# Optimization experiments

Hardware: AMD Instinct MI355X
Metric: run time of the kernel (lower is better)

The kernel has to match this reference:

```python
import jax, jax.numpy as jnp
import numpy as np

B, T, H, IN, D = 256, 64, 256, 2, 8

def _gru_cell(x, h, Wih, Whh, bih, bhh):
    gi = x @ Wih.T + bih          # [B,3H]
    gh = h @ Whh.T + bhh
    ir, iz, inn = jnp.split(gi, 3, axis=-1)
    hr, hz, hn = jnp.split(gh, 3, axis=-1)
    r = jax.nn.sigmoid(ir + hr)
    z = jax.nn.sigmoid(iz + hz)
    n = jnp.tanh(inn + r * hn)
    return (1.0 - z) * n + z * h

def _gru2(x, h, p):
    # h: [2,B,H]; p: 8-tuple of layer-0 then layer-1 GRU params
    h0 = _gru_cell(x, h[0], p[0], p[1], p[2], p[3])
    h1 = _gru_cell(h0, h[1], p[4], p[5], p[6], p[7])
    return jnp.stack([h0, h1], axis=0)

def _attend(h_new, buf, i, attn_W, v_W, fc_W, fc_b):
    # h_new: [2,B,H] fresh RNN hidden; buf: [B,T,2,H] history of hiddens
    s = h_new.transpose(1, 0, 2)                            # [B,2,H]
    es = jnp.einsum('blh,gh->blg', s, attn_W[:, :H])        # s half of cat(s,hiddens)
    eh = jnp.einsum('bjlh,gh->bjlg', buf, attn_W[:, H:])    # hiddens half
    energy = jnp.tanh(es[:, None] + eh)                     # [B,T,2,H]
    logits = jnp.einsum('bjlg,og->bjlo', energy, v_W)       # [B,T,2,2]
    mask = (jnp.arange(buf.shape[1]) <= i)[None, :, None, None]
    logits = jnp.where(mask, logits, jnp.float32(-1e30))
    m = logits.max(axis=(1, 2), keepdims=True)              # softmax over all 2*(i+1) history slots
    e = jnp.exp(logits - m)
    a = e / e.sum(axis=(1, 2), keepdims=True)
    c = jnp.einsum('bjlo,bjlh->obh', a, buf)                # [2,B,H] == bmm(a,hiddens).transpose(0,1)
    h_cat = jnp.concatenate([c, h_new], axis=-1)            # [2,B,2H]
    return h_cat @ fc_W.T + fc_b                            # [2,B,H]

def setup_inputs():
    key = jax.random.key(0)
    ks = jax.random.split(key, 32)
    def u(k, shape, fan):
        b = 1.0 / np.sqrt(fan)
        return jax.random.uniform(k, shape, jnp.float32, -b, b)
    inp = {'received': jax.random.normal(ks[0], (B, T, IN), jnp.float32)}
    i = 1
    for g in ('g1', 'g2'):
        inp[g + '_Wih0'] = u(ks[i], (3 * H, IN), H); i += 1
        inp[g + '_Whh0'] = u(ks[i], (3 * H, H), H); i += 1
        inp[g + '_bih0'] = u(ks[i], (3 * H,), H); i += 1
        inp[g + '_bhh0'] = u(ks[i], (3 * H,), H); i += 1
        inp[g + '_Wih1'] = u(ks[i], (3 * H, H), H); i += 1
        inp[g + '_Whh1'] = u(ks[i], (3 * H, H), H); i += 1
        inp[g + '_bih1'] = u(ks[i], (3 * H,), H); i += 1
        inp[g + '_bhh1'] = u(ks[i], (3 * H,), H); i += 1
    inp['fc_W'] = u(ks[i], (H, 2 * H), 2 * H); i += 1
    inp['fc_b'] = u(ks[i], (H,), 2 * H); i += 1
    inp['attn_W'] = u(ks[i], (H, 2 * H), 2 * H); i += 1
    inp['v_W'] = u(ks[i], (2, H), H); i += 1
    inp['out_W'] = u(ks[i], (1, 2 * H), 2 * H); i += 1
    inp['out_b'] = u(ks[i], (1,), 2 * H); i += 1
    return inp

def reference(received, g1_Wih0, g1_Whh0, g1_bih0, g1_bhh0, g1_Wih1, g1_Whh1, g1_bih1, g1_bhh1,
              g2_Wih0, g2_Whh0, g2_bih0, g2_bhh0, g2_Wih1, g2_Whh1, g2_bih1, g2_bhh1,
              fc_W, fc_b, attn_W, v_W, out_W, out_b):
    p1 = (g1_Wih0, g1_Whh0, g1_bih0, g1_bhh0, g1_Wih1, g1_Whh1, g1_bih1, g1_bhh1)
    p2 = (g2_Wih0, g2_Whh0, g2_bih0, g2_bhh0, g2_Wih1, g2_Whh1, g2_bih1, g2_bhh1)
    b, t = received.shape[0], received.shape[1]
    h_init = jnp.zeros((2, b, H), received.dtype)
    buf_init = jnp.zeros((b, t, 2, H), received.dtype)

    def step(carry, inp):
        h1, h2, b1, b2 = carry
        x, i = inp
        h1n = _gru2(x, h1, p1)
        h2n = _gru2(x, h2, p2)
        b1 = b1.at[:, i].set(h1n.transpose(1, 0, 2))
        b2 = b2.at[:, i].set(h2n.transpose(1, 0, 2))
        h1a = _attend(h1n, b1, i, attn_W, v_W, fc_W, fc_b)
        h2a = _attend(h2n, b2, i, attn_W, v_W, fc_W, fc_b)
        return (h1a, h2a, b1, b2), (h1n[1], h2n[1])

    xs = (received.transpose(1, 0, 2), jnp.arange(t))
    _, (o1, o2) = jax.lax.scan(step, (h_init, h_init, buf_init, buf_init), xs)
    out1 = o1.transpose(1, 0, 2)   # [B,T,H] = concat of per-step top-layer GRU outputs
    out2 = o2.transpose(1, 0, 2)
    ar = jnp.arange(t)
    idx = jnp.where(ar >= t - D - 1, t - 1, ar + D)   # delayed stream-2 features
    rnn_out = jnp.concatenate([out1, out2[:, idx]], axis=-1)  # [B,T,2H]
    return jax.nn.sigmoid(rnn_out @ out_W.T + out_b)          # [B,T,1]
```

## Files before the change

### kernel.cpp

```cpp
#include <hip/hip_runtime.h>

#define BATCH 256
#define TT    64
#define HH    256
#define DD    8

#define BW    4
#define NTHR  1024
#define NBLK  (2 * (BATCH / BW))

typedef __attribute__((ext_vector_type(8))) short bfrag;
typedef __attribute__((ext_vector_type(4))) float f4;
typedef unsigned int uint_t;
typedef __attribute__((ext_vector_type(4))) unsigned int uv4;

#define SWZ(g) ((((g) & 31) << 3) | ((g) >> 5))

__device__ __forceinline__ float rcpf(float x) { return __builtin_amdgcn_rcpf(x); }
__device__ __forceinline__ float sigf(float x) { return rcpf(1.0f + __expf(-x)); }
__device__ __forceinline__ float tanh_fast(float x) {
  const float e = __expf(-2.0f * x);
  return __builtin_fmaf(2.0f, rcpf(1.0f + e), -1.0f);
}
__device__ __forceinline__ unsigned short f2bf(float f) {
  union { float f; unsigned int u; } v; v.f = f;
  return (unsigned short)((v.u + 0x7fffu + ((v.u >> 16) & 1u)) >> 16);
}
__device__ __forceinline__ float bf_lo(unsigned int u) {
  union { unsigned int u; float f; } v; v.u = u << 16; return v.f;
}
__device__ __forceinline__ float bf_hi(unsigned int u) {
  union { unsigned int u; float f; } v; v.u = u & 0xffff0000u; return v.f;
}
__device__ __forceinline__ bfrag zero_frag() {
  bfrag r;
#pragma unroll
  for (int x = 0; x < 8; x++) r[x] = 0;
  return r;
}
__device__ __forceinline__ f4 mfma16(bfrag a, bfrag b, f4 c) {
  return __builtin_amdgcn_mfma_f32_16x16x32_bf16(a, b, c, 0, 0, 0);
}

#define W1_ELEMS  196608
#define STACK_W   (3 * W1_ELEMS)
#define B3_OFF    (2 * STACK_W)
#define B4_OFF    (B3_OFF + 131072)
#define WF_TOTAL  (B4_OFF + 131072)

__global__ __launch_bounds__(256) void prep_weights(
    const float* __restrict__ g1_Whh0, const float* __restrict__ g1_Wih1, const float* __restrict__ g1_Whh1,
    const float* __restrict__ g2_Whh0, const float* __restrict__ g2_Wih1, const float* __restrict__ g2_Whh1,
    const float* __restrict__ attn_W, const float* __restrict__ fc_W,
    unsigned short* __restrict__ wf) {
  const int id = blockIdx.x * 256 + threadIdx.x;
  if (id >= WF_TOTAL) return;
  float src;
  if (id < 2 * STACK_W) {
    const int s = id / STACK_W, r = id % STACK_W;
    const int mm = r / W1_ELEMS, e = r % W1_ELEMS;
    const int j = e & 7, lane = (e >> 3) & 63, c = (e >> 9) & 7, t = e >> 12;
    const int nt = t / 3, g = t % 3;
    const int n = nt * 16 + (lane & 15);
    const int k = c * 32 + ((lane >> 4) << 3) + j;
    const float* W = (mm == 0) ? (s ? g2_Whh0 : g1_Whh0)
                   : (mm == 1) ? (s ? g2_Wih1 : g1_Wih1)
                               : (s ? g2_Whh1 : g1_Whh1);
    src = W[(g * 256 + n) * 256 + k];
  } else if (id < B4_OFF) {
    const int e = id - B3_OFF;
    const int j = e & 7, lane = (e >> 3) & 63, c = (e >> 9) & 7, t = e >> 12;
    const int n = t * 16 + (lane & 15);
    const int k = c * 32 + ((lane >> 4) << 3) + j;
    src = (n < 256) ? attn_W[n * 512 + k] : attn_W[(n - 256) * 512 + 256 + k];
  } else {
    const int e = id - B4_OFF;
    const int j = e & 7, lane = (e >> 3) & 63, c = (e >> 9) & 15, t = e >> 13;
    const int n = t * 16 + (lane & 15);
    const int k = c * 32 + ((lane >> 4) << 3) + j;
    src = fc_W[n * 512 + k];
  }
  wf[id] = f2bf(src);
}

__global__ __launch_bounds__(NTHR, 4) void gru_attn(
    const float* __restrict__ received,
    const float* __restrict__ g1_Wih0, const float* __restrict__ g1_bih0, const float* __restrict__ g1_bhh0,
    const float* __restrict__ g1_bih1, const float* __restrict__ g1_bhh1,
    const float* __restrict__ g2_Wih0, const float* __restrict__ g2_bih0, const float* __restrict__ g2_bhh0,
    const float* __restrict__ g2_bih1, const float* __restrict__ g2_bhh1,
    const float* __restrict__ fc_b, const float* __restrict__ v_W, const float* __restrict__ out_W,
    const unsigned short* __restrict__ wf,
    unsigned short* __restrict__ buf_g, unsigned short* __restrict__ ehb_g,
    float* __restrict__ ws_p) {
  const int tid  = threadIdx.x;
  const int lane = tid & 63, wave = tid >> 6;
  const int col  = lane & 15, q = lane >> 4;
  const int s    = blockIdx.x & 1;
  const int b0   = (blockIdx.x >> 1) * BW;

  const float* Wih0 = s ? g2_Wih0 : g1_Wih0;
  const float* bih0 = s ? g2_bih0 : g1_bih0;
  const float* bhh0 = s ? g2_bhh0 : g1_bhh0;
  const float* bih1 = s ? g2_bih1 : g1_bih1;
  const float* bhh1 = s ? g2_bhh1 : g1_bhh1;

  const bfrag* W1  = (const bfrag*)(wf + (size_t)s * STACK_W);
  const bfrag* W2I = W1 + W1_ELEMS / 8;
  const bfrag* W2H = W2I + W1_ELEMS / 8;
  const bfrag* B3  = (const bfrag*)(wf + B3_OFF);
  const bfrag* B4  = (const bfrag*)(wf + B4_OFF);

  unsigned short* buf = buf_g + (size_t)s * BATCH * TT * 2 * HH;
  unsigned short* ehb = ehb_g + (size_t)s * BATCH * TT * 2 * HH;
  float* pp = ws_p + (size_t)s * BATCH * TT;

  const int nm = wave * 16 + col;
  const float wxr0 = Wih0[nm * 2],         wxr1 = Wih0[nm * 2 + 1];
  const float wxz0 = Wih0[(256 + nm) * 2], wxz1 = Wih0[(256 + nm) * 2 + 1];
  const float wxn0 = Wih0[(512 + nm) * 2], wxn1 = Wih0[(512 + nm) * 2 + 1];
  const float br0  = bih0[nm] + bhh0[nm];
  const float bz0  = bih0[256 + nm] + bhh0[256 + nm];
  const float bni0 = bih0[512 + nm], bnh0 = bhh0[512 + nm];
  const float br1  = bih1[nm] + bhh1[nm];
  const float bz1  = bih1[256 + nm] + bhh1[256 + nm];
  const float bni1 = bih1[512 + nm], bnh1 = bhh1[512 + nm];
  const float fcbv = fc_b[nm];
  const float owv  = out_W[s * HH + nm];

  __shared__ float          hf[8 * 260] __attribute__((aligned(16)));
  __shared__ unsigned short hb[8 * 264] __attribute__((aligned(16)));
  __shared__ unsigned short hnb[8 * 264] __attribute__((aligned(16)));
  __shared__ float          es_s[8 * 264] __attribute__((aligned(16)));
  __shared__ unsigned short cacb[8 * 264] __attribute__((aligned(16)));
  __shared__ float          lp[TT * 4 * 2 * 2];
  __shared__ float          vw_s[512];
  __shared__ float          cpart[2 * 2 * 4 * 256];
  __shared__ float          pw_s[64];
  __shared__ float          sinv_s[8];

  for (int x = tid; x < 8 * 260; x += NTHR) hf[x] = 0.0f;
  for (int x = tid; x < 8 * 264; x += NTHR) hb[x] = 0;
  if (tid < 512) { const int o = tid >> 8, g = tid & 255; vw_s[o * 256 + SWZ(g)] = v_W[tid]; }
  __syncthreads();

#pragma unroll 1
  for (int i = 0; i < TT; ++i) {
    float2 xv[BW];
#pragma unroll
    for (int b = 0; b < BW; b++) xv[b] = ((const float2*)received)[(size_t)(b0 + b) * TT + i];

    {
      f4 aR = {0, 0, 0, 0}, aZ = {0, 0, 0, 0}, aN = {0, 0, 0, 0};
#pragma unroll
      for (int c = 0; c < 8; c++) {
        const bfrag a = (col < BW) ? *(const bfrag*)&hb[col * 264 + c * 32 + q * 8] : zero_frag();
        aR = mfma16(a, W1[((wave * 3 + 0) * 8 + c) * 64 + lane], aR);
        aZ = mfma16(a, W1[((wave * 3 + 1) * 8 + c) * 64 + lane], aZ);
        aN = mfma16(a, W1[((wave * 3 + 2) * 8 + c) * 64 + lane], aN);
      }
      if (lane < 16) {
#pragma unroll
        for (int reg = 0; reg < 4; reg++) {
          const int b = reg;
          const float r  = sigf(xv[b].x * wxr0 + xv[b].y * wxr1 + br0 + aR[reg]);
          const float z  = sigf(xv[b].x * wxz0 + xv[b].y * wxz1 + bz0 + aZ[reg]);
          const float nn = tanh_fast(xv[b].x * wxn0 + xv[b].y * wxn1 + bni0 + r * (aN[reg] + bnh0));
          const float hn0 = (1.0f - z) * nn + z * hf[b * 260 + nm];
          const unsigned short hv = f2bf(hn0);
          hnb[b * 264 + nm] = hv;
          buf[((size_t)(b0 + b) * (TT * 2) + i * 2 + 0) * HH + nm] = hv;
        }
      }
    }
    __syncthreads();

    {
      f4 iR = {0,0,0,0}, iZ = {0,0,0,0}, iN = {0,0,0,0};
      f4 hR = {0,0,0,0}, hZ = {0,0,0,0}, hN = {0,0,0,0};
#pragma unroll
      for (int c = 0; c < 8; c++) {
        const bfrag ai = (col < BW) ? *(const bfrag*)&hnb[col * 264 + c * 32 + q * 8] : zero_frag();
        const bfrag ah = (col < BW) ? *(const bfrag*)&hb[(4 + col) * 264 + c * 32 + q * 8] : zero_frag();
        iR = mfma16(ai, W2I[((wave * 3 + 0) * 8 + c) * 64 + lane], iR);
        iZ = mfma16(ai, W2I[((wave * 3 + 1) * 8 + c) * 64 + lane], iZ);
        iN = mfma16(ai, W2I[((wave * 3 + 2) * 8 + c) * 64 + lane], iN);
        hR = mfma16(ah, W2H[((wave * 3 + 0) * 8 + c) * 64 + lane], hR);
        hZ = mfma16(ah, W2H[((wave * 3 + 1) * 8 + c) * 64 + lane], hZ);
        hN = mfma16(ah, W2H[((wave * 3 + 2) * 8 + c) * 64 + lane], hN);
      }
      float pv[4] = {0.f, 0.f, 0.f, 0.f};
      if (lane < 16) {
#pragma unroll
        for (int reg = 0; reg < 4; reg++) {
          const int b = reg;
          const float r  = sigf(iR[reg] + hR[reg] + br1);
          const float z  = sigf(iZ[reg] + hZ[reg] + bz1);
          const float nn = tanh_fast(iN[reg] + bni1 + r * (hN[reg] + bnh1));
          const float hn1 = (1.0f - z) * nn + z * hf[(4 + b) * 260 + nm];
          const unsigned short hv = f2bf(hn1);
          hnb[(4 + b) * 264 + nm] = hv;
          buf[((size_t)(b0 + b) * (TT * 2) + i * 2 + 1) * HH + nm] = hv;
          pv[reg] = hn1 * owv;
        }
      }
#pragma unroll
      for (int reg = 0; reg < 4; reg++) {
#pragma unroll
        for (int d = 1; d < 16; d <<= 1) pv[reg] += __shfl_xor(pv[reg], d, 64);
      }
      if (lane == 0) {
#pragma unroll
        for (int reg = 0; reg < 4; reg++) pw_s[wave * 4 + reg] = pv[reg];
      }
    }
    __syncthreads();

    {
#pragma unroll
      for (int tt = 0; tt < 2; tt++) {
        const int t = wave * 2 + tt;
        f4 acc = {0, 0, 0, 0};
#pragma unroll
        for (int c = 0; c < 8; c++) {
          const bfrag a = (col < 8) ? *(const bfrag*)&hnb[col * 264 + c * 32 + q * 8] : zero_frag();
          acc = mfma16(a, B3[(t * 8 + c) * 64 + lane], acc);
        }
        if (lane < 32) {
          const int n = t * 16 + col;
#pragma unroll
          for (int reg = 0; reg < 4; reg++) {
            const int m = q * 4 + reg;
            const int l = m >> 2, b = m & 3;
            if (t < 16) es_s[(b * 2 + l) * 264 + SWZ(n)] = acc[reg];
            else ehb[((size_t)(b0 + b) * (TT * 2) + i * 2 + l) * HH + (n - 256)] = f2bf(acc[reg]);
          }
        }
      }
      if (tid < 4) {
        float ss = 0.0f;
#pragma unroll
        for (int w = 0; w < 16; w++) ss += pw_s[w * 4 + tid];
        pp[(size_t)(b0 + tid) * TT + i] = ss;
      }
    }
    __syncthreads();

    {
      const int nslot = 64 * (i + 1);
      for (int slot = tid; slot < nslot; slot += NTHR) {
        const int g8 = slot & 7;
        const int b  = (slot >> 3) & 3;
        const int l  = (slot >> 5) & 1;
        const int j  = slot >> 6;
        const uv4* ep = (const uv4*)(ehb + ((size_t)(b0 + b) * (TT * 2) + j * 2 + l) * HH + g8 * 32);
        const int eb = (b * 2 + l) * 264;
        float l0 = 0.0f, l1 = 0.0f;
#pragma unroll
        for (int u = 0; u < 4; u++) {
          const uv4 uu = __builtin_nontemporal_load(ep + u);
#pragma unroll
          for (int k = 0; k < 4; k++) {
            const int m = u * 8 + k * 2;
            const float e0 = tanh_fast(es_s[eb + (m * 8 + g8)] + bf_lo(uu[k]));
            const float e1 = tanh_fast(es_s[eb + ((m + 1) * 8 + g8)] + bf_hi(uu[k]));
            l0 = fmaf(e0, vw_s[m * 8 + g8], fmaf(e1, vw_s[(m + 1) * 8 + g8], l0));
            l1 = fmaf(e0, vw_s[256 + m * 8 + g8], fmaf(e1, vw_s[256 + (m + 1) * 8 + g8], l1));
          }
        }
#pragma unroll
        for (int d = 1; d < 8; d <<= 1) { l0 += __shfl_xor(l0, d, 64); l1 += __shfl_xor(l1, d, 64); }
        if (g8 == 0) {
          lp[((j * 4 + b) * 2 + l) * 2 + 0] = __expf(l0);
          lp[((j * 4 + b) * 2 + l) * 2 + 1] = __expf(l1);
        }
      }
    }
    __syncthreads();

    {
      if (wave < 8) {
        const int b = wave >> 1, o = wave & 1;
        float sa = 0.0f;
        if (lane <= i)
          sa = lp[((lane * 4 + b) * 2 + 0) * 2 + o] + lp[((lane * 4 + b) * 2 + 1) * 2 + o];
#pragma unroll
        for (int d = 1; d < 64; d <<= 1) sa += __shfl_xor(sa, d, 64);
        if (lane == 0) sinv_s[b * 2 + o] = rcpf(sa);
      }
      const int b = tid >> 8, jh = (tid >> 7) & 1, h2 = tid & 127;
      const uint_t* bp = (const uint_t*)(buf + ((size_t)(b0 + b) * (TT * 2)) * HH) + h2;
      float c00 = 0.f, c01 = 0.f, c10 = 0.f, c11 = 0.f;
      for (int j = jh; j <= i; j += 2) {
#pragma unroll
        for (int l = 0; l < 2; l++) {
          const uint_t u = __builtin_nontemporal_load(bp + (j * 2 + l) * 128);
          const float e0 = lp[((j * 4 + b) * 2 + l) * 2 + 0];
          const float e1 = lp[((j * 4 + b) * 2 + l) * 2 + 1];
          const float v0 = bf_lo(u), v1 = bf_hi(u);
          c00 = fmaf(e0, v0, c00); c01 = fmaf(e0, v1, c01);
          c10 = fmaf(e1, v0, c10); c11 = fmaf(e1, v1, c11);
        }
      }
      float* cp0 = &cpart[((jh * 2 + 0) * 4 + b) * 256 + h2 * 2];
      cp0[0] = c00; cp0[1] = c01;
      float* cp1 = &cpart[((jh * 2 + 1) * 4 + b) * 256 + h2 * 2];
      cp1[0] = c10; cp1[1] = c11;
    }
    __syncthreads();

    {
#pragma unroll
      for (int r = 0; r < 2; r++) {
        const int idx = tid + r * NTHR;
        const int o = idx >> 10, b = (idx >> 8) & 3, h = idx & 255;
        const float v = (cpart[(o * 4 + b) * 256 + h] + cpart[((2 + o) * 4 + b) * 256 + h]) *
                        sinv_s[b * 2 + o];
        cacb[(o * 4 + b) * 264 + h] = f2bf(v);
      }
    }
    __syncthreads();

    {
      f4 acc = {0, 0, 0, 0};
#pragma unroll
      for (int c = 0; c < 16; c++) {
        bfrag a;
        if (col < 8) {
          if (c < 8) a = *(const bfrag*)&cacb[col * 264 + c * 32 + q * 8];
          else       a = *(const bfrag*)&hnb[col * 264 + (c - 8) * 32 + q * 8];
        } else a = zero_frag();
        acc = mfma16(a, B4[(wave * 16 + c) * 64 + lane], acc);
      }
      if (lane < 32) {
#pragma unroll
        for (int reg = 0; reg < 4; reg++) {
          const int m = q * 4 + reg;
          const float v = acc[reg] + fcbv;
          hf[m * 260 + nm] = v;
          hb[m * 264 + nm] = f2bf(v);
        }
      }
    }
    __syncthreads();
  }
}

__global__ __launch_bounds__(256) void final_combine(const float* __restrict__ ws_p,
                                                     const float* __restrict__ out_b,
                                                     float* __restrict__ out) {
  const int gidx = blockIdx.x * blockDim.x + threadIdx.x;
  if (gidx >= BATCH * TT) return;
  const int b = gidx >> 6;
  const int t = gidx & 63;
  const int idx = (t >= TT - DD - 1) ? (TT - 1) : (t + DD);
  const float* p1 = ws_p;
  const float* p2 = ws_p + (size_t)BATCH * TT;
  const float v = p1[(size_t)b * TT + t] + p2[(size_t)b * TT + idx] + out_b[0];
  out[gidx] = 1.0f / (1.0f + __expf(-v));
}

extern "C" void kernel_launch(void* const* d_in, const int* in_sizes, int n_in,
                              void* d_out, int out_size, void* d_ws, size_t ws_size,
                              hipStream_t stream) {
  const float* received = (const float*)d_in[0];
  const float* g1_Wih0 = (const float*)d_in[1];
  const float* g1_Whh0 = (const float*)d_in[2];
  const float* g1_bih0 = (const float*)d_in[3];
  const float* g1_bhh0 = (const float*)d_in[4];
  const float* g1_Wih1 = (const float*)d_in[5];
  const float* g1_Whh1 = (const float*)d_in[6];
  const float* g1_bih1 = (const float*)d_in[7];
  const float* g1_bhh1 = (const float*)d_in[8];
  const float* g2_Wih0 = (const float*)d_in[9];
  const float* g2_Whh0 = (const float*)d_in[10];
  const float* g2_bih0 = (const float*)d_in[11];
  const float* g2_bhh0 = (const float*)d_in[12];
  const float* g2_Wih1 = (const float*)d_in[13];
  const float* g2_Whh1 = (const float*)d_in[14];
  const float* g2_bih1 = (const float*)d_in[15];
  const float* g2_bhh1 = (const float*)d_in[16];
  const float* fc_W   = (const float*)d_in[17];
  const float* fc_b   = (const float*)d_in[18];
  const float* attn_W = (const float*)d_in[19];
  const float* v_W    = (const float*)d_in[20];
  const float* out_W  = (const float*)d_in[21];
  const float* out_b  = (const float*)d_in[22];

  float* ws_p = (float*)d_ws;
  unsigned short* buf = (unsigned short*)(ws_p + 2 * BATCH * TT);
  unsigned short* ehb = buf + (size_t)2 * BATCH * TT * 2 * HH;
  unsigned short* wf  = ehb + (size_t)2 * BATCH * TT * 2 * HH;

  hipLaunchKernelGGL(prep_weights, dim3((WF_TOTAL + 255) / 256), dim3(256), 0, stream,
                     g1_Whh0, g1_Wih1, g1_Whh1, g2_Whh0, g2_Wih1, g2_Whh1,
                     attn_W, fc_W, wf);

  hipLaunchKernelGGL(gru_attn, dim3(NBLK), dim3(NTHR), 0, stream,
                     received,
                     g1_Wih0, g1_bih0, g1_bhh0, g1_bih1, g1_bhh1,
                     g2_Wih0, g2_bih0, g2_bhh0, g2_bih1, g2_bhh1,
                     fc_b, v_W, out_W, wf, buf, ehb, ws_p);

  hipLaunchKernelGGL(final_combine, dim3((BATCH * TT + 255) / 256), dim3(256), 0, stream,
                     ws_p, out_b, (float*)d_out);
}
```

Measured before the change: 6.185 ms.

## Halve block size, give each wave two tiles, prefetch weights and history loads

Blocks shrink from 1024 to 512 threads, so each wave now covers two output tiles in the GRU, energy and fc stages. The A fragments are hoisted into registers, and all B fragments for a tile are loaded before its MFMAs run. The energy loop and the context accumulation now software-prefetch the next ehb/buf chunk, and the context loop uses wider uv2 loads. The aim is to hide global-load latency and lower barrier cost per wave, at the price of more registers per thread and fewer waves per block.

After: 5.926 ms. -4.2%, faster.

```diff
diff --git a/kernel.cpp b/kernel.cpp
--- a/kernel.cpp
+++ b/kernel.cpp
@@ -6,13 +6,13 @@
 #define DD    8
 
 #define BW    4
-#define NTHR  1024
+#define NTHR  512
 #define NBLK  (2 * (BATCH / BW))
 
 typedef __attribute__((ext_vector_type(8))) short bfrag;
 typedef __attribute__((ext_vector_type(4))) float f4;
-typedef unsigned int uint_t;
 typedef __attribute__((ext_vector_type(4))) unsigned int uv4;
+typedef __attribute__((ext_vector_type(2))) unsigned int uv2;
 
 #define SWZ(g) ((((g) & 31) << 3) | ((g) >> 5))
 
@@ -83,7 +83,7 @@
   wf[id] = f2bf(src);
 }
 
-__global__ __launch_bounds__(NTHR, 4) void gru_attn(
+__global__ __launch_bounds__(NTHR, 2) void gru_attn(
     const float* __restrict__ received,
     const float* __restrict__ g1_Wih0, const float* __restrict__ g1_bih0, const float* __restrict__ g1_bhh0,
     const float* __restrict__ g1_bih1, const float* __restrict__ g1_bhh1,
@@ -115,18 +115,25 @@
   unsigned short* ehb = ehb_g + (size_t)s * BATCH * TT * 2 * HH;
   float* pp = ws_p + (size_t)s * BATCH * TT;
 
-  const int nm = wave * 16 + col;
-  const float wxr0 = Wih0[nm * 2],         wxr1 = Wih0[nm * 2 + 1];
-  const float wxz0 = Wih0[(256 + nm) * 2], wxz1 = Wih0[(256 + nm) * 2 + 1];
-  const float wxn0 = Wih0[(512 + nm) * 2], wxn1 = Wih0[(512 + nm) * 2 + 1];
-  const float br0  = bih0[nm] + bhh0[nm];
-  const float bz0  = bih0[256 + nm] + bhh0[256 + nm];
-  const float bni0 = bih0[512 + nm], bnh0 = bhh0[512 + nm];
-  const float br1  = bih1[nm] + bhh1[nm];
-  const float bz1  = bih1[256 + nm] + bhh1[256 + nm];
-  const float bni1 = bih1[512 + nm], bnh1 = bhh1[512 + nm];
-  const float fcbv = fc_b[nm];
-  const float owv  = out_W[s * HH + nm];
+  float wxr0v[2], wxr1v[2], wxz0v[2], wxz1v[2], wxn0v[2], wxn1v[2];
+  float br0v[2], bz0v[2], bni0v[2], bnh0v[2];
+  float br1v[2], bz1v[2], bni1v[2], bnh1v[2];
+  float fcbv[2], owvv[2];
+#pragma unroll
+  for (int r2 = 0; r2 < 2; r2++) {
+    const int nm = (wave + 8 * r2) * 16 + col;
+    wxr0v[r2] = Wih0[nm * 2];         wxr1v[r2] = Wih0[nm * 2 + 1];
+    wxz0v[r2] = Wih0[(256 + nm) * 2]; wxz1v[r2] = Wih0[(256 + nm) * 2 + 1];
+    wxn0v[r2] = Wih0[(512 + nm) * 2]; wxn1v[r2] = Wih0[(512 + nm) * 2 + 1];
+    br0v[r2]  = bih0[nm] + bhh0[nm];
+    bz0v[r2]  = bih0[256 + nm] + bhh0[256 + nm];
+    bni0v[r2] = bih0[512 + nm]; bnh0v[r2] = bhh0[512 + nm];
+    br1v[r2]  = bih1[nm] + bhh1[nm];
+    bz1v[r2]  = bih1[256 + nm] + bhh1[256 + nm];
+    bni1v[r2] = bih1[512 + nm]; bnh1v[r2] = bhh1[512 + nm];
+    fcbv[r2]  = fc_b[nm];
+    owvv[r2]  = out_W[s * HH + nm];
+  }
 
   __shared__ float          hf[8 * 260] __attribute__((aligned(16)));
   __shared__ unsigned short hb[8 * 264] __attribute__((aligned(16)));
@@ -135,13 +142,13 @@
   __shared__ unsigned short cacb[8 * 264] __attribute__((aligned(16)));
   __shared__ float          lp[TT * 4 * 2 * 2];
   __shared__ float          vw_s[512];
-  __shared__ float          cpart[2 * 2 * 4 * 256];
-  __shared__ float          pw_s[64];
+  __shared__ float          cpart[2 * 2 * 4 * 256] __attribute__((aligned(16)));
+  __shared__ float          pw_s[32];
   __shared__ float          sinv_s[8];
 
   for (int x = tid; x < 8 * 260; x += NTHR) hf[x] = 0.0f;
   for (int x = tid; x < 8 * 264; x += NTHR) hb[x] = 0;
-  if (tid < 512) { const int o = tid >> 8, g = tid & 255; vw_s[o * 256 + SWZ(g)] = v_W[tid]; }
+  { const int o = tid >> 8, g = tid & 255; vw_s[o * 256 + SWZ(g)] = v_W[tid]; }
   __syncthreads();
 
 #pragma unroll 1
@@ -151,81 +158,126 @@
     for (int b = 0; b < BW; b++) xv[b] = ((const float2*)received)[(size_t)(b0 + b) * TT + i];
 
     {
-      f4 aR = {0, 0, 0, 0}, aZ = {0, 0, 0, 0}, aN = {0, 0, 0, 0};
+      bfrag a0[8];
+#pragma unroll
+      for (int c = 0; c < 8; c++)
+        a0[c] = (col < BW) ? *(const bfrag*)&hb[col * 264 + c * 32 + q * 8] : zero_frag();
+#pragma unroll
+      for (int r2 = 0; r2 < 2; r2++) {
+        const int nt16 = wave + 8 * r2;
+        bfrag bb[24];
+#pragma unroll
+        for (int c = 0; c < 8; c++) {
+          bb[c]      = W1[((nt16 * 3 + 0) * 8 + c) * 64 + lane];
+          bb[8 + c]  = W1[((nt16 * 3 + 1) * 8 + c) * 64 + lane];
+          bb[16 + c] = W1[((nt16 * 3 + 2) * 8 + c) * 64 + lane];
+        }
+        f4 aR = {0, 0, 0, 0}, aZ = {0, 0, 0, 0}, aN = {0, 0, 0, 0};
+#pragma unroll
+        for (int c = 0; c < 8; c++) {
+          aR = mfma16(a0[c], bb[c], aR);
+          aZ = mfma16(a0[c], bb[8 + c], aZ);
+          aN = mfma16(a0[c], bb[16 + c], aN);
+        }
+        if (lane < 16) {
+          const int nm = nt16 * 16 + col;
+#pragma unroll
+          for (int reg = 0; reg < 4; reg++) {
+            const int b = reg;
+            const float rr = sigf(xv[b].x * wxr0v[r2] + xv[b].y * wxr1v[r2] + br0v[r2] + aR[reg]);
+            const float zz = sigf(xv[b].x * wxz0v[r2] + xv[b].y * wxz1v[r2] + bz0v[r2] + aZ[reg]);
+            const float nn = tanh_fast(xv[b].x * wxn0v[r2] + xv[b].y * wxn1v[r2] + bni0v[r2] +
+                                       rr * (aN[reg] + bnh0v[r2]));
+            const float hn0 = (1.0f - zz) * nn + zz * hf[b * 260 + nm];
+            const unsigned short hv = f2bf(hn0);
+            hnb[b * 264 + nm] = hv;
+            buf[((size_t)(b0 + b) * (TT * 2) + i * 2 + 0) * HH + nm] = hv;
+          }
+        }
+      }
+    }
+    __syncthreads();
+
+    {
+      bfrag ai[8], ah[8];
 #pragma unroll
       for (int c = 0; c < 8; c++) {
-        const bfrag a = (col < BW) ? *(const bfrag*)&hb[col * 264 + c * 32 + q * 8] : zero_frag();
-        aR = mfma16(a, W1[((wave * 3 + 0) * 8 + c) * 64 + lane], aR);
-        aZ = mfma16(a, W1[((wave * 3 + 1) * 8 + c) * 64 + lane], aZ);
-        aN = mfma16(a, W1[((wave * 3 + 2) * 8 + c) * 64 + lane], aN);
-      }
-      if (lane < 16) {
-#pragma unroll
-        for (int reg = 0; reg < 4; reg++) {
-          const int b = reg;
-          const float r  = sigf(xv[b].x * wxr0 + xv[b].y * wxr1 + br0 + aR[reg]);
-          const float z  = sigf(xv[b].x * wxz0 + xv[b].y * wxz1 + bz0 + aZ[reg]);
-          const float nn = tanh_fast(xv[b].x * wxn0 + xv[b].y * wxn1 + bni0 + r * (aN[reg] + bnh0));
-          const float hn0 = (1.0f - z) * nn + z * hf[b * 260 + nm];
-          const unsigned short hv = f2bf(hn0);
-          hnb[b * 264 + nm] = hv;
-          buf[((size_t)(b0 + b) * (TT * 2) + i * 2 + 0) * HH + nm] = hv;
-        }
+        ai[c] = (col < BW) ? *(const bfrag*)&hnb[col * 264 + c * 32 + q * 8] : zero_frag();
+        ah[c] = (col < BW) ? *(const bfrag*)&hb[(4 + col) * 264 + c * 32 + q * 8] : zero_frag();
+      }
+      float pv[4] = {0.f, 0.f, 0.f, 0.f};
+#pragma unroll
+      for (int r2 = 0; r2 < 2; r2++) {
+        const int nt16 = wave + 8 * r2;
+        bfrag bb[24];
+#pragma unroll
+        for (int c = 0; c < 8; c++) {
+          bb[c]      = W2I[((nt16 * 3 + 0) * 8 + c) * 64 + lane];
+          bb[8 + c]  = W2I[((nt16 * 3 + 1) * 8 + c) * 64 + lane];
+          bb[16 + c] = W2I[((nt16 * 3 + 2) * 8 + c) * 64 + lane];
+        }
+        f4 iR = {0, 0, 0, 0}, iZ = {0, 0, 0, 0}, iN = {0, 0, 0, 0};
+#pragma unroll
+        for (int c = 0; c < 8; c++) {
+          iR = mfma16(ai[c], bb[c], iR);
+          iZ = mfma16(ai[c], bb[8 + c], iZ);
+          iN = mfma16(ai[c], bb[16 + c], iN);
+        }
+#pragma unroll
+        for (int c = 0; c < 8; c++) {
+          bb[c]      = W2H[((nt16 * 3 + 0) * 8 + c) * 64 + lane];
+          bb[8 + c]  = W2H[((nt16 * 3 + 1) * 8 + c) * 64 + lane];
+          bb[16 + c] = W2H[((nt16 * 3 + 2) * 8 + c) * 64 + lane];
+        }
+        f4 hR = {0, 0, 0, 0}, hZ = {0, 0, 0, 0}, hN = {0, 0, 0, 0};
+#pragma unroll
+        for (int c = 0; c < 8; c++) {
+          hR = mfma16(ah[c], bb[c], hR);
+          hZ = mfma16(ah[c], bb[8 + c], hZ);
+          hN = mfma16(ah[c], bb[16 + c], hN);
+        }
+        if (lane < 16) {
+          const int nm = nt16 * 16 + col;
+#pragma unroll
+          for (int reg = 0; reg < 4; reg++) {
+            const int b = reg;
+            const float rr = sigf(iR[reg] + hR[reg] + br1v[r2]);
+            const float zz = sigf(iZ[reg] + hZ[reg] + bz1v[r2]);
+            const float nn = tanh_fast(iN[reg] + bni1v[r2] + rr * (hN[reg] + bnh1v[r2]));
+            const float hn1 = (1.0f - zz) * nn + zz * hf[(4 + b) * 260 + nm];
+            const unsigned short hv = f2bf(hn1);
+            hnb[(4 + b) * 264 + nm] = hv;
+            buf[((size_t)(b0 + b) * (TT * 2) + i * 2 + 1) * HH + nm] = hv;
+            pv[reg] += hn1 * owvv[r2];
+          }
+        }
+      }
+#pragma unroll
+      for (int reg = 0; reg < 4; reg++) {
+#pragma unroll
+        for (int d = 1; d < 16; d <<= 1) pv[reg] += __shfl_xor(pv[reg], d, 64);
+      }
+      if (lane == 0) {
+#pragma unroll
+        for (int reg = 0; reg < 4; reg++) pw_s[wave * 4 + reg] = pv[reg];
       }
     }
     __syncthreads();
 
     {
-      f4 iR = {0,0,0,0}, iZ = {0,0,0,0}, iN = {0,0,0,0};
-      f4 hR = {0,0,0,0}, hZ = {0,0,0,0}, hN = {0,0,0,0};
-#pragma unroll
-      for (int c = 0; c < 8; c++) {
-        const bfrag ai = (col < BW) ? *(const bfrag*)&hnb[col * 264 + c * 32 + q * 8] : zero_frag();
-        const bfrag ah = (col < BW) ? *(const bfrag*)&hb[(4 + col) * 264 + c * 32 + q * 8] : zero_frag();
-        iR = mfma16(ai, W2I[((wave * 3 + 0) * 8 + c) * 64 + lane], iR);
-        iZ = mfma16(ai, W2I[((wave * 3 + 1) * 8 + c) * 64 + lane], iZ);
-        iN = mfma16(ai, W2I[((wave * 3 + 2) * 8 + c) * 64 + lane], iN);
-        hR = mfma16(ah, W2H[((wave * 3 + 0) * 8 + c) * 64 + lane], hR);
-        hZ = mfma16(ah, W2H[((wave * 3 + 1) * 8 + c) * 64 + lane], hZ);
-        hN = mfma16(ah, W2H[((wave * 3 + 2) * 8 + c) * 64 + lane], hN);
-      }
-      float pv[4] = {0.f, 0.f, 0.f, 0.f};
-      if (lane < 16) {
-#pragma unroll
-        for (int reg = 0; reg < 4; reg++) {
-          const int b = reg;
-          const float r  = sigf(iR[reg] + hR[reg] + br1);
-          const float z  = sigf(iZ[reg] + hZ[reg] + bz1);
-          const float nn = tanh_fast(iN[reg] + bni1 + r * (hN[reg] + bnh1));
-          const float hn1 = (1.0f - z) * nn + z * hf[(4 + b) * 260 + nm];
-          const unsigned short hv = f2bf(hn1);
-          hnb[(4 + b) * 264 + nm] = hv;
-          buf[((size_t)(b0 + b) * (TT * 2) + i * 2 + 1) * HH + nm] = hv;
-          pv[reg] = hn1 * owv;
-        }
-      }
-#pragma unroll
-      for (int reg = 0; reg < 4; reg++) {
-#pragma unroll
-        for (int d = 1; d < 16; d <<= 1) pv[reg] += __shfl_xor(pv[reg], d, 64);
-      }
-      if (lane == 0) {
-#pragma unroll
-        for (int reg = 0; reg < 4; reg++) pw_s[wave * 4 + reg] = pv[reg];
-      }
-    }
-    __syncthreads();
-
-    {
-#pragma unroll
-      for (int tt = 0; tt < 2; tt++) {
-        const int t = wave * 2 + tt;
+      bfrag a3[8];
+#pragma unroll
+      for (int c = 0; c < 8; c++)
+        a3[c] = (col < 8) ? *(const bfrag*)&hnb[col * 264 + c * 32 + q * 8] : zero_frag();
+#pragma unroll
+      for (int tt = 0; tt < 4; tt++) {
+        const int t = wave * 4 + tt;
+        bfrag bb[8];
+#pragma unroll
+        for (int c = 0; c < 8; c++) bb[c] = B3[(t * 8 + c) * 64 + lane];
         f4 acc = {0, 0, 0, 0};
 #pragma unroll
-        for (int c = 0; c < 8; c++) {
-          const bfrag a = (col < 8) ? *(const bfrag*)&hnb[col * 264 + c * 32 + q * 8] : zero_frag();
-          acc = mfma16(a, B3[(t * 8 + c) * 64 + lane], acc);
-        }
+        for (int c = 0; c < 8; c++) acc = mfma16(a3[c], bb[c], acc);
         if (lane < 32) {
           const int n = t * 16 + col;
 #pragma unroll
@@ -240,7 +292,7 @@
       if (tid < 4) {
         float ss = 0.0f;
 #pragma unroll
-        for (int w = 0; w < 16; w++) ss += pw_s[w * 4 + tid];
+        for (int w = 0; w < 8; w++) ss += pw_s[w * 4 + tid];
         pp[(size_t)(b0 + tid) * TT + i] = ss;
       }
     }
@@ -248,22 +300,39 @@
 
     {
       const int nslot = 64 * (i + 1);
-      for (int slot = tid; slot < nslot; slot += NTHR) {
+      int slot = tid;
+      uv4 cur[4];
+      if (slot < nslot) {
+        const uv4* ep = (const uv4*)(ehb + ((size_t)(b0 + ((slot >> 3) & 3)) * (TT * 2) +
+                                            (slot >> 6) * 2 + ((slot >> 5) & 1)) * HH + (slot & 7) * 32);
+#pragma unroll
+        for (int u = 0; u < 4; u++) cur[u] = __builtin_nontemporal_load(ep + u);
+      }
+      for (; slot < nslot; slot += NTHR) {
+        const int snext = slot + NTHR;
+        uv4 nxt[4];
+        if (snext < nslot) {
+          const uv4* ep2 = (const uv4*)(ehb + ((size_t)(b0 + ((snext >> 3) & 3)) * (TT * 2) +
+                                               (snext >> 6) * 2 + ((snext >> 5) & 1)) * HH + (snext & 7) * 32);
+#pragma unroll
+          for (int u = 0; u < 4; u++) nxt[u] = __builtin_nontemporal_load(ep2 + u);
+        } else {
+#pragma unroll
+          for (int u = 0; u < 4; u++) nxt[u] = cur[u];
+        }
         const int g8 = slot & 7;
         const int b  = (slot >> 3) & 3;
         const int l  = (slot >> 5) & 1;
         const int j  = slot >> 6;
-        const uv4* ep = (const uv4*)(ehb + ((size_t)(b0 + b) * (TT * 2) + j * 2 + l) * HH + g8 * 32);
         const int eb = (b * 2 + l) * 264;
         float l0 = 0.0f, l1 = 0.0f;
 #pragma unroll
         for (int u = 0; u < 4; u++) {
-          const uv4 uu = __builtin_nontemporal_load(ep + u);
 #pragma unroll
           for (int k = 0; k < 4; k++) {
             const int m = u * 8 + k * 2;
-            const float e0 = tanh_fast(es_s[eb + (m * 8 + g8)] + bf_lo(uu[k]));
-            const float e1 = tanh_fast(es_s[eb + ((m + 1) * 8 + g8)] + bf_hi(uu[k]));
+            const float e0 = tanh_fast(es_s[eb + (m * 8 + g8)] + bf_lo(cur[u][k]));
+            const float e1 = tanh_fast(es_s[eb + ((m + 1) * 8 + g8)] + bf_hi(cur[u][k]));
             l0 = fmaf(e0, vw_s[m * 8 + g8], fmaf(e1, vw_s[(m + 1) * 8 + g8], l0));
             l1 = fmaf(e0, vw_s[256 + m * 8 + g8], fmaf(e1, vw_s[256 + (m + 1) * 8 + g8], l1));
           }
@@ -274,71 +343,101 @@
           lp[((j * 4 + b) * 2 + l) * 2 + 0] = __expf(l0);
           lp[((j * 4 + b) * 2 + l) * 2 + 1] = __expf(l1);
         }
+#pragma unroll
+        for (int u = 0; u < 4; u++) cur[u] = nxt[u];
       }
     }
     __syncthreads();
 
     {
-      if (wave < 8) {
+      {
         const int b = wave >> 1, o = wave & 1;
+        const int jl2 = 2 * (i + 1);
+        const int jl0 = lane, jl1 = lane + 64;
         float sa = 0.0f;
-        if (lane <= i)
-          sa = lp[((lane * 4 + b) * 2 + 0) * 2 + o] + lp[((lane * 4 + b) * 2 + 1) * 2 + o];
+        if (jl0 < jl2) sa += lp[((jl0 >> 1) * 4 + b) * 4 + (jl0 & 1) * 2 + o];
+        if (jl1 < jl2) sa += lp[((jl1 >> 1) * 4 + b) * 4 + (jl1 & 1) * 2 + o];
 #pragma unroll
         for (int d = 1; d < 64; d <<= 1) sa += __shfl_xor(sa, d, 64);
         if (lane == 0) sinv_s[b * 2 + o] = rcpf(sa);
       }
-      const int b = tid >> 8, jh = (tid >> 7) & 1, h2 = tid & 127;
-      const uint_t* bp = (const uint_t*)(buf + ((size_t)(b0 + b) * (TT * 2)) * HH) + h2;
-      float c00 = 0.f, c01 = 0.f, c10 = 0.f, c11 = 0.f;
-      for (int j = jh; j <= i; j += 2) {
+      const int h4   = tid & 63;
+      const int jpar = (tid >> 6) & 1;
+      const int cb   = tid >> 7;
+      const uv2* bp = (const uv2*)(buf + ((size_t)(b0 + cb) * (TT * 2)) * HH);
+      float c00 = 0.f, c01 = 0.f, c02 = 0.f, c03 = 0.f;
+      float c10 = 0.f, c11 = 0.f, c12 = 0.f, c13 = 0.f;
+      uv2 aj0 = {0, 0}, aj1 = {0, 0}, bj0 = {0, 0}, bj1 = {0, 0};
+      int j = jpar;
+      if (j <= i) {
+        aj0 = __builtin_nontemporal_load(bp + (j * 2 + 0) * 64 + h4);
+        aj1 = __builtin_nontemporal_load(bp + (j * 2 + 1) * 64 + h4);
+        bj0 = __builtin_nontemporal_load(bp + ((j + 2) * 2 + 0) * 64 + h4);
+        bj1 = __builtin_nontemporal_load(bp + ((j + 2) * 2 + 1) * 64 + h4);
+      }
+      for (; j <= i; j += 2) {
+        uv2 cj0 = {0, 0}, cj1 = {0, 0};
+        if (j + 4 <= i) {
+          cj0 = __builtin_nontemporal_load(bp + ((j + 4) * 2 + 0) * 64 + h4);
+          cj1 = __builtin_nontemporal_load(bp + ((j + 4) * 2 + 1) * 64 + h4);
+        }
 #pragma unroll
         for (int l = 0; l < 2; l++) {
-          const uint_t u = __builtin_nontemporal_load(bp + (j * 2 + l) * 128);
-          const float e0 = lp[((j * 4 + b) * 2 + l) * 2 + 0];
-          const float e1 = lp[((j * 4 + b) * 2 + l) * 2 + 1];
-          const float v0 = bf_lo(u), v1 = bf_hi(u);
+          const uv2 u = l ? aj1 : aj0;
+          const float e0 = lp[((j * 4 + cb) * 2 + l) * 2 + 0];
+          const float e1 = lp[((j * 4 + cb) * 2 + l) * 2 + 1];
+          const float v0 = bf_lo(u[0]), v1 = bf_hi(u[0]);
+          const float v2 = bf_lo(u[1]), v3 = bf_hi(u[1]);
           c00 = fmaf(e0, v0, c00); c01 = fmaf(e0, v1, c01);
+          c02 = fmaf(e0, v2, c02); c03 = fmaf(e0, v3, c03);
           c10 = fmaf(e1, v0, c10); c11 = fmaf(e1, v1, c11);
-        }
-      }
-      float* cp0 = &cpart[((jh * 2 + 0) * 4 + b) * 256 + h2 * 2];
-      cp0[0] = c00; cp0[1] = c01;
-      float* cp1 = &cpart[((jh * 2 + 1) * 4 + b) * 256 + h2 * 2];
-      cp1[0] = c10; cp1[1] = c11;
+          c12 = fmaf(e1, v2, c12); c13 = fmaf(e1, v3, c13);
+        }
+        aj0 = bj0; aj1 = bj1; bj0 = cj0; bj1 = cj1;
+      }
+      ((float4*)&cpart[((jpar * 2 + 0) * 4 + cb) * 256])[h4] = make_float4(c00, c01, c02, c03);
+      ((float4*)&cpart[((jpar * 2 + 1) * 4 + cb) * 256])[h4] = make_float4(c10, c11, c12, c13);
+    }
+    __syncthreads();
+
+    for (int x = tid; x < 2 * BW * HH; x += NTHR) {
+      const int g = x & 255, b = (x >> 8) & 3, o = x >> 10;
+      const float v = (cpart[(o * 4 + b) * 256 + g] + cpart[((2 + o) * 4 + b) * 256 + g]) *
+                      sinv_s[b * 2 + o];
+      cacb[(o * 4 + b) * 264 + g] = f2bf(v);
     }
     __syncthreads();
 
     {
-#pragma unroll
-      for (int r = 0; r < 2; r++) {
-        const int idx = tid + r * NTHR;
-        const int o = idx >> 10, b = (idx >> 8) & 3, h = idx & 255;
-        const float v = (cpart[(o * 4 + b) * 256 + h] + cpart[((2 + o) * 4 + b) * 256 + h]) *
-                        sinv_s[b * 2 + o];
-        cacb[(o * 4 + b) * 264 + h] = f2bf(v);
-      }
-    }
-    __syncthreads();
-
-    {
-      f4 acc = {0, 0, 0, 0};
-#pragma unroll
-      for (int c = 0; c < 16; c++) {
-        bfrag a;
-        if (col < 8) {
-          if (c < 8) a = *(const bfrag*)&cacb[col * 264 + c * 32 + q * 8];
-          else       a = *(const bfrag*)&hnb[col * 264 + (c - 8) * 32 + q * 8];
-        } else a = zero_frag();
-        acc = mfma16(a, B4[(wave * 16 + c) * 64 + lane], acc);
-      }
-      if (lane < 32) {
-#pragma unroll
-        for (int reg = 0; reg < 4; reg++) {
-          const int m = q * 4 + reg;
-          const float v = acc[reg] + fcbv;
-          hf[m * 260 + nm] = v;
-          hb[m * 264 + nm] = f2bf(v);
+      bfrag a4[16];
+      if (col < 8) {
+#pragma unroll
+        for (int c = 0; c < 8; c++) {
+          a4[c]     = *(const bfrag*)&cacb[col * 264 + c * 32 + q * 8];
+          a4[c + 8] = *(const bfrag*)&hnb[col * 264 + c * 32 + q * 8];
+        }
+      } else {
+#pragma unroll
+        for (int c = 0; c < 16; c++) a4[c] = zero_frag();
+      }
+#pragma unroll
+      for (int r2 = 0; r2 < 2; r2++) {
+        const int t16 = wave + 8 * r2;
+        bfrag bb[16];
+#pragma unroll
+        for (int c = 0; c < 16; c++) bb[c] = B4[(t16 * 16 + c) * 64 + lane];
+        f4 acc = {0, 0, 0, 0};
+#pragma unroll
+        for (int c = 0; c < 16; c++) acc = mfma16(a4[c], bb[c], acc);
+        if (lane < 32) {
+          const int nm = t16 * 16 + col;
+#pragma unroll
+          for (int reg = 0; reg < 4; reg++) {
+            const int m = q * 4 + reg;
+            const float v = acc[reg] + fcbv[r2];
+            hf[m * 260 + nm] = v;
+            hb[m * 264 + nm] = f2bf(v);
+          }
         }
       }
     }
```
